# Optimization experiments

Measured on AMD Instinct MI355X. Metric: run time of the kernel, lower is better.

The kernel has to match this reference:

```python
import jax, jax.numpy as jnp
import numpy as np

ACT_BITS = 7      # activation - 1 (symmetric signed quantization)
WEIGHT_BITS = 7   # weight - 1
LN_EPS = 1e-5


def t_quantize(x, k):
    # Symmetric per-tensor uniform quantization to k bits with STE.
    # q = round(clip(x/s, -1, 1) * (2^k - 1)) / (2^k - 1) * s, s = max|x|
    n = float(2 ** k - 1)
    s = jnp.maximum(jnp.max(jnp.abs(x)), 1e-12)
    q = jnp.round(jnp.clip(x / s, -1.0, 1.0) * n) / n * s
    return x + jax.lax.stop_gradient(q - x)  # straight-through


def layer_norm(x, gamma, beta):
    mu = jnp.mean(x, axis=-1, keepdims=True)
    var = jnp.mean(jnp.square(x - mu), axis=-1, keepdims=True)
    return (x - mu) * jax.lax.rsqrt(var + LN_EPS) * gamma + beta


def ir_linear(x, w, b):
    # IRlinear: linear with per-tensor quantized weights (STE).
    wq = t_quantize(w, WEIGHT_BITS)
    return jnp.einsum('bsd,hd->bsh', x, wq) + b


def setup_inputs() -> dict:
    key = jax.random.key(0)
    ks = jax.random.split(key, 4)
    dim, hidden = 1024, 4096
    B, S = 4, 8192
    return {
        'x': jax.random.normal(ks[0], (B, S, dim), dtype=jnp.float32),
        'gamma': jnp.ones((dim,), jnp.float32),
        'beta': jnp.zeros((dim,), jnp.float32),
        'w1': jax.random.normal(ks[1], (hidden, dim), jnp.float32) * (1.0 / np.sqrt(dim)),
        'b1': jnp.zeros((hidden,), jnp.float32),
        'w2': jax.random.normal(ks[2], (dim, hidden), jnp.float32) * (1.0 / np.sqrt(hidden)),
        'b2': jnp.zeros((dim,), jnp.float32),
    }


def reference(x, gamma, beta, w1, b1, w2, b2):
    # x = T_quantize(LayerNorm(x), activation-1)
    h = t_quantize(layer_norm(x, gamma, beta), ACT_BITS)
    # x = T_quantize(GELU(IRlinear1(x)), activation-1)  (exact erf GELU, torch default)
    h = t_quantize(jax.nn.gelu(ir_linear(h, w1, b1), approximate=False), ACT_BITS)
    # net[3:] = Dropout(0) -> IRlinear2 -> Dropout(0)
    return ir_linear(h, w2, b2)
```

## Files before the change

### kernel.cpp

```cpp
#include <hip/hip_runtime.h>
#include <stdint.h>

typedef int v4i __attribute__((ext_vector_type(4)));

#define GLD_LDS16(g, l) __builtin_amdgcn_global_load_lds( \
    (const __attribute__((address_space(1))) void*)(g),   \
    (__attribute__((address_space(3))) void*)(l), 16, 0, 0)

__device__ __forceinline__ float wsum(float v){
  #pragma unroll
  for (int o = 32; o; o >>= 1) v += __shfl_xor(v, o, 64);
  return v;
}
__device__ __forceinline__ float wmaxr(float v){
  #pragma unroll
  for (int o = 32; o; o >>= 1) v = fmaxf(v, __shfl_xor(v, o, 64));
  return v;
}
__device__ __forceinline__ float gelu_f(float x){
  return 0.5f * x * (1.0f + erff(x * 0.7071067811865476f));
}

__global__ __launch_bounds__(256) void k_ln_absmax(
    const float* __restrict__ x, const float* __restrict__ gamma,
    const float* __restrict__ beta, unsigned int* __restrict__ smax_out, int M)
{
  __shared__ float red[4];
  const int lane = threadIdx.x & 63, wave = threadIdx.x >> 6;
  float lmax = 0.f;
  for (int row = blockIdx.x * 4 + wave; row < M; row += gridDim.x * 4) {
    const float4* xr = (const float4*)(x + (size_t)row * 1024);
    float4 v[4]; float s = 0.f;
    #pragma unroll
    for (int j = 0; j < 4; j++){ v[j] = xr[j*64 + lane]; s += v[j].x+v[j].y+v[j].z+v[j].w; }
    s = wsum(s);
    const float mu = s * (1.f/1024.f);
    float sq = 0.f;
    #pragma unroll
    for (int j = 0; j < 4; j++){
      float a=v[j].x-mu, b=v[j].y-mu, c=v[j].z-mu, d=v[j].w-mu;
      sq += a*a + b*b + c*c + d*d;
    }
    sq = wsum(sq);
    const float rs = 1.0f / sqrtf(sq * (1.f/1024.f) + 1e-5f);
    #pragma unroll
    for (int j = 0; j < 4; j++){
      int c0 = j*256 + lane*4;
      float4 g = *(const float4*)(gamma + c0);
      float4 b = *(const float4*)(beta + c0);
      float y0=(v[j].x-mu)*rs*g.x+b.x, y1=(v[j].y-mu)*rs*g.y+b.y;
      float y2=(v[j].z-mu)*rs*g.z+b.z, y3=(v[j].w-mu)*rs*g.w+b.w;
      lmax = fmaxf(lmax, fmaxf(fmaxf(fabsf(y0),fabsf(y1)), fmaxf(fabsf(y2),fabsf(y3))));
    }
  }
  lmax = wmaxr(lmax);
  if (lane == 0) red[wave] = lmax;
  __syncthreads();
  if (threadIdx.x == 0)
    atomicMax(smax_out, __float_as_uint(fmaxf(fmaxf(red[0],red[1]), fmaxf(red[2],red[3]))));
}

__global__ __launch_bounds__(256) void k_ln_quant(
    const float* __restrict__ x, const float* __restrict__ gamma,
    const float* __restrict__ beta, const unsigned int* __restrict__ sbits,
    signed char* __restrict__ A1, int M)
{
  const float s = fmaxf(__uint_as_float(*sbits), 1e-12f);
  const int lane = threadIdx.x & 63, wave = threadIdx.x >> 6;
  for (int row = blockIdx.x * 4 + wave; row < M; row += gridDim.x * 4) {
    const float4* xr = (const float4*)(x + (size_t)row * 1024);
    float4 v[4]; float sm = 0.f;
    #pragma unroll
    for (int j = 0; j < 4; j++){ v[j] = xr[j*64 + lane]; sm += v[j].x+v[j].y+v[j].z+v[j].w; }
    sm = wsum(sm);
    const float mu = sm * (1.f/1024.f);
    float sq = 0.f;
    #pragma unroll
    for (int j = 0; j < 4; j++){
      float a=v[j].x-mu, b=v[j].y-mu, c=v[j].z-mu, d=v[j].w-mu;
      sq += a*a + b*b + c*c + d*d;
    }
    sq = wsum(sq);
    const float rs = 1.0f / sqrtf(sq * (1.f/1024.f) + 1e-5f);
    #pragma unroll
    for (int j = 0; j < 4; j++){
      int c0 = j*256 + lane*4;
      float4 g = *(const float4*)(gamma + c0);
      float4 b = *(const float4*)(beta + c0);
      float y0=(v[j].x-mu)*rs*g.x+b.x, y1=(v[j].y-mu)*rs*g.y+b.y;
      float y2=(v[j].z-mu)*rs*g.z+b.z, y3=(v[j].w-mu)*rs*g.w+b.w;
      char4 qc;
      qc.x = (signed char)(int)rintf(fminf(fmaxf(y0/s,-1.f),1.f)*127.f);
      qc.y = (signed char)(int)rintf(fminf(fmaxf(y1/s,-1.f),1.f)*127.f);
      qc.z = (signed char)(int)rintf(fminf(fmaxf(y2/s,-1.f),1.f)*127.f);
      qc.w = (signed char)(int)rintf(fminf(fmaxf(y3/s,-1.f),1.f)*127.f);
      *(char4*)(A1 + (size_t)row*1024 + c0) = qc;
    }
  }
}

__global__ __launch_bounds__(256) void k_absmax(
    const float* __restrict__ w, long n4, unsigned int* __restrict__ out)
{
  __shared__ float red[4];
  const int lane = threadIdx.x & 63, wave = threadIdx.x >> 6;
  float lmax = 0.f;
  for (long i = blockIdx.x*256 + threadIdx.x; i < n4; i += (long)gridDim.x*256) {
    float4 v = ((const float4*)w)[i];
    lmax = fmaxf(lmax, fmaxf(fmaxf(fabsf(v.x),fabsf(v.y)), fmaxf(fabsf(v.z),fabsf(v.w))));
  }
  lmax = wmaxr(lmax);
  if (lane == 0) red[wave] = lmax;
  __syncthreads();
  if (threadIdx.x == 0)
    atomicMax(out, __float_as_uint(fmaxf(fmaxf(red[0],red[1]), fmaxf(red[2],red[3]))));
}

__global__ __launch_bounds__(256) void k_wquant(
    const float* __restrict__ w, long n4, const unsigned int* __restrict__ sbits,
    signed char* __restrict__ wq)
{
  const float s = fmaxf(__uint_as_float(*sbits), 1e-12f);
  for (long i = blockIdx.x*256 + threadIdx.x; i < n4; i += (long)gridDim.x*256) {
    float4 v = ((const float4*)w)[i];
    char4 qc;
    qc.x = (signed char)(int)rintf(fminf(fmaxf(v.x/s,-1.f),1.f)*127.f);
    qc.y = (signed char)(int)rintf(fminf(fmaxf(v.y/s,-1.f),1.f)*127.f);
    qc.z = (signed char)(int)rintf(fminf(fmaxf(v.z/s,-1.f),1.f)*127.f);
    qc.w = (signed char)(int)rintf(fminf(fmaxf(v.w/s,-1.f),1.f)*127.f);
    *(char4*)(wq + i*4) = qc;
  }
}

template<int MODE>
__global__ __launch_bounds__(256, 4) void k_gemm_i8(
    const signed char* __restrict__ A, const signed char* __restrict__ W,
    const float* __restrict__ bias, const unsigned int* __restrict__ scales,
    float* __restrict__ outf, signed char* __restrict__ outq,
    unsigned int* __restrict__ gmax,
    int M, int N, int K, int ia, int iw, int ig)
{
  __shared__ __align__(16) signed char As[128*64];
  __shared__ __align__(16) signed char Bs[128*64];
  __shared__ float red[4];

  const int nwg = gridDim.x, orig = blockIdx.x;
  const int q8 = nwg >> 3, r8 = nwg & 7;
  const int xcd = orig & 7, idx = orig >> 3;
  const int wgid = (xcd < r8 ? xcd*(q8+1) : r8*(q8+1) + (xcd-r8)*q8) + idx;

  const int tn = N >> 7;
  const int bm = wgid / tn, bn = wgid % tn;
  const int tid = threadIdx.x, lane = tid & 63, wave = tid >> 6;
  const int wm = wave >> 1, wn = wave & 1;
  const size_t row0 = (size_t)bm * 128, col0 = (size_t)bn * 128;

  v4i acc[4][4];
  #pragma unroll
  for (int i = 0; i < 4; i++)
    #pragma unroll
    for (int j = 0; j < 4; j++) acc[i][j] = (v4i){0,0,0,0};

  int st_r[2], st_kk[2];
  #pragma unroll
  for (int i = 0; i < 2; i++) {
    const int chunk = i*4 + wave;
    const int off = chunk*1024 + lane*16;
    const int r = off >> 6;
    const int c = (off >> 4) & 3;
    st_r[i]  = r;
    st_kk[i] = (c ^ ((r >> 1) & 3)) << 4;
  }

  const int ksteps = K >> 6;
  for (int kt = 0; kt < ksteps; ++kt) {
    const size_t kb = (size_t)kt << 6;
    #pragma unroll
    for (int i = 0; i < 2; i++) {
      const int chunk = i*4 + wave;
      GLD_LDS16(A + (row0 + st_r[i])*(size_t)K + kb + st_kk[i], As + chunk*1024);
      GLD_LDS16(W + (col0 + st_r[i])*(size_t)K + kb + st_kk[i], Bs + chunk*1024);
    }
    __syncthreads();

    v4i af[4], bf[4];
    const int cfrag = lane >> 4;
    #pragma unroll
    for (int mi = 0; mi < 4; mi++) {
      const int rr = wm*64 + mi*16 + (lane & 15);
      af[mi] = *(const v4i*)(As + (rr << 6) + ((cfrag ^ ((rr >> 1) & 3)) << 4));
    }
    #pragma unroll
    for (int ni = 0; ni < 4; ni++) {
      const int rr = wn*64 + ni*16 + (lane & 15);
      bf[ni] = *(const v4i*)(Bs + (rr << 6) + ((cfrag ^ ((rr >> 1) & 3)) << 4));
    }
    #pragma unroll
    for (int mi = 0; mi < 4; mi++)
      #pragma unroll
      for (int ni = 0; ni < 4; ni++)
        acc[mi][ni] = __builtin_amdgcn_mfma_i32_16x16x64_i8(af[mi], bf[ni], acc[mi][ni], 0, 0, 0);
    __syncthreads();
  }

  const float sa = fmaxf(__uint_as_float(scales[ia]), 1e-12f);
  const float sw = fmaxf(__uint_as_float(scales[iw]), 1e-12f);
  const float sc = (sa / 127.f) * (sw / 127.f);
  const int rowbase = (int)row0 + wm*64;
  const int colbase = (int)col0 + wn*64;

  if (MODE == 0) {
    float lmax = 0.f;
    #pragma unroll
    for (int mi = 0; mi < 4; mi++)
      #pragma unroll
      for (int ni = 0; ni < 4; ni++) {
        const int colc = colbase + ni*16 + (lane & 15);
        const float b = bias[colc];
        #pragma unroll
        for (int j = 0; j < 4; j++) {
          float g = gelu_f((float)acc[mi][ni][j] * sc + b);
          lmax = fmaxf(lmax, fabsf(g));
        }
      }
    lmax = wmaxr(lmax);
    if (lane == 0) red[wave] = lmax;
    __syncthreads();
    if (tid == 0)
      atomicMax(gmax, __float_as_uint(fmaxf(fmaxf(red[0],red[1]), fmaxf(red[2],red[3]))));
  } else if (MODE == 1) {
    const float sg = fmaxf(__uint_as_float(scales[ig]), 1e-12f);
    #pragma unroll
    for (int mi = 0; mi < 4; mi++)
      #pragma unroll
      for (int ni = 0; ni < 4; ni++) {
        const int colc = colbase + ni*16 + (lane & 15);
        const float b = bias[colc];
        #pragma unroll
        for (int j = 0; j < 4; j++) {
          const int row = rowbase + mi*16 + ((lane >> 4) << 2) + j;
          float g = gelu_f((float)acc[mi][ni][j] * sc + b);
          float t = fminf(fmaxf(g / sg, -1.f), 1.f) * 127.f;
          outq[(size_t)row * N + colc] = (signed char)(int)rintf(t);
        }
      }
  } else {
    #pragma unroll
    for (int mi = 0; mi < 4; mi++)
      #pragma unroll
      for (int ni = 0; ni < 4; ni++) {
        const int colc = colbase + ni*16 + (lane & 15);
        const float b = bias[colc];
        #pragma unroll
        for (int j = 0; j < 4; j++) {
          const int row = rowbase + mi*16 + ((lane >> 4) << 2) + j;
          outf[(size_t)row * N + colc] = (float)acc[mi][ni][j] * sc + b;
        }
      }
  }
}

extern "C" void kernel_launch(void* const* d_in, const int* in_sizes, int n_in,
                              void* d_out, int out_size, void* d_ws, size_t ws_size,
                              hipStream_t stream)
{
  const float* x     = (const float*)d_in[0];
  const float* gamma = (const float*)d_in[1];
  const float* beta  = (const float*)d_in[2];
  const float* w1    = (const float*)d_in[3];
  const float* b1    = (const float*)d_in[4];
  const float* w2    = (const float*)d_in[5];
  const float* b2    = (const float*)d_in[6];
  float* out = (float*)d_out;

  const int D = 1024;
  const int M = in_sizes[0] / D;
  const int H = in_sizes[3] / D;

  char* ws = (char*)d_ws;
  unsigned int* scales = (unsigned int*)ws;
  signed char* A1  = (signed char*)(ws + 256);
  signed char* w1q = A1 + (size_t)M * D;
  signed char* w2q = w1q + (size_t)H * D;
  signed char* A2  = w2q + (size_t)H * D;

  hipMemsetAsync(scales, 0, 32, stream);
  k_absmax<<<512, 256, 0, stream>>>(w1, (long)H * D / 4, scales + 1);
  k_absmax<<<512, 256, 0, stream>>>(w2, (long)H * D / 4, scales + 2);
  k_ln_absmax<<<4096, 256, 0, stream>>>(x, gamma, beta, scales, M);
  k_wquant<<<512, 256, 0, stream>>>(w1, (long)H * D / 4, scales + 1, w1q);
  k_wquant<<<512, 256, 0, stream>>>(w2, (long)H * D / 4, scales + 2, w2q);
  k_ln_quant<<<4096, 256, 0, stream>>>(x, gamma, beta, scales, A1, M);

  const int g1 = (M / 128) * (H / 128);
  k_gemm_i8<0><<<g1, 256, 0, stream>>>(A1, w1q, b1, scales, nullptr, nullptr,
                                       scales + 3, M, H, D, 0, 1, 0);
  k_gemm_i8<1><<<g1, 256, 0, stream>>>(A1, w1q, b1, scales, nullptr, A2,
                                       nullptr, M, H, D, 0, 1, 3);
  const int g2 = (M / 128) * (D / 128);
  k_gemm_i8<2><<<g2, 256, 0, stream>>>(A2, w2q, b2, scales, out, nullptr,
                                       nullptr, M, D, H, 3, 2, 0);
}
```

Measured before the change: 1.182 ms.

## Double-buffer LDS tiles in int8 GEMM to overlap global loads with MFMA

Splits the A and W shared-memory tiles into two buffers. The next K-slice is prefetched with global_load_lds while MFMAs run on the current slice, and the per-iteration barrier pair becomes a single vmcnt wait plus barrier. MFMA sections are wrapped in s_setprio to favour the compute waves. This doubles LDS use per block and lowers the launch-bounds occupancy hint from 4 to 2, which may cut the number of resident waves available to hide latency.

```diff
diff --git a/kernel.cpp b/kernel.cpp
--- a/kernel.cpp
+++ b/kernel.cpp
@@ -133,15 +133,15 @@
 }
 
 template<int MODE>
-__global__ __launch_bounds__(256, 4) void k_gemm_i8(
+__global__ __launch_bounds__(256, 2) void k_gemm_i8(
     const signed char* __restrict__ A, const signed char* __restrict__ W,
     const float* __restrict__ bias, const unsigned int* __restrict__ scales,
     float* __restrict__ outf, signed char* __restrict__ outq,
     unsigned int* __restrict__ gmax,
     int M, int N, int K, int ia, int iw, int ig)
 {
-  __shared__ __align__(16) signed char As[128*64];
-  __shared__ __align__(16) signed char Bs[128*64];
+  __shared__ __align__(16) signed char As[2][128*64];
+  __shared__ __align__(16) signed char Bs[2][128*64];
   __shared__ float red[4];
 
   const int nwg = gridDim.x, orig = blockIdx.x;
@@ -161,7 +161,7 @@
     #pragma unroll
     for (int j = 0; j < 4; j++) acc[i][j] = (v4i){0,0,0,0};
 
-  int st_r[2], st_kk[2];
+  int st_r[2], st_kk[2], st_ch[2];
   #pragma unroll
   for (int i = 0; i < 2; i++) {
     const int chunk = i*4 + wave;
@@ -170,38 +170,55 @@
     const int c = (off >> 4) & 3;
     st_r[i]  = r;
     st_kk[i] = (c ^ ((r >> 1) & 3)) << 4;
-  }
+    st_ch[i] = chunk*1024;
+  }
+  const signed char* Ab = A + row0 * (size_t)K;
+  const signed char* Wb = W + col0 * (size_t)K;
+
+  #define STAGE(buf, kb_) do {                                              \
+    _Pragma("unroll")                                                       \
+    for (int i_ = 0; i_ < 2; i_++) {                                        \
+      GLD_LDS16(Ab + (size_t)st_r[i_]*K + (kb_) + st_kk[i_], As[buf] + st_ch[i_]); \
+      GLD_LDS16(Wb + (size_t)st_r[i_]*K + (kb_) + st_kk[i_], Bs[buf] + st_ch[i_]); \
+    }                                                                       \
+  } while (0)
 
   const int ksteps = K >> 6;
+  STAGE(0, 0);
+  asm volatile("s_waitcnt vmcnt(0)");
+  __builtin_amdgcn_s_barrier();
+
+  int cur = 0;
   for (int kt = 0; kt < ksteps; ++kt) {
-    const size_t kb = (size_t)kt << 6;
-    #pragma unroll
-    for (int i = 0; i < 2; i++) {
-      const int chunk = i*4 + wave;
-      GLD_LDS16(A + (row0 + st_r[i])*(size_t)K + kb + st_kk[i], As + chunk*1024);
-      GLD_LDS16(W + (col0 + st_r[i])*(size_t)K + kb + st_kk[i], Bs + chunk*1024);
-    }
-    __syncthreads();
+    if (kt + 1 < ksteps) STAGE(cur ^ 1, (size_t)(kt + 1) << 6);
 
     v4i af[4], bf[4];
     const int cfrag = lane >> 4;
     #pragma unroll
     for (int mi = 0; mi < 4; mi++) {
       const int rr = wm*64 + mi*16 + (lane & 15);
-      af[mi] = *(const v4i*)(As + (rr << 6) + ((cfrag ^ ((rr >> 1) & 3)) << 4));
+      af[mi] = *(const v4i*)(As[cur] + (rr << 6) + ((cfrag ^ ((rr >> 1) & 3)) << 4));
     }
     #pragma unroll
     for (int ni = 0; ni < 4; ni++) {
       const int rr = wn*64 + ni*16 + (lane & 15);
-      bf[ni] = *(const v4i*)(Bs + (rr << 6) + ((cfrag ^ ((rr >> 1) & 3)) << 4));
-    }
+      bf[ni] = *(const v4i*)(Bs[cur] + (rr << 6) + ((cfrag ^ ((rr >> 1) & 3)) << 4));
+    }
+    __builtin_amdgcn_s_setprio(1);
     #pragma unroll
     for (int mi = 0; mi < 4; mi++)
       #pragma unroll
       for (int ni = 0; ni < 4; ni++)
         acc[mi][ni] = __builtin_amdgcn_mfma_i32_16x16x64_i8(af[mi], bf[ni], acc[mi][ni], 0, 0, 0);
-    __syncthreads();
-  }
+    __builtin_amdgcn_s_setprio(0);
+
+    if (kt + 1 < ksteps) {
+      asm volatile("s_waitcnt vmcnt(0)");
+      __builtin_amdgcn_s_barrier();
+      cur ^= 1;
+    }
+  }
+  #undef STAGE
 
   const float sa = fmaxf(__uint_as_float(scales[ia]), 1e-12f);
   const float sw = fmaxf(__uint_as_float(scales[iw]), 1e-12f);
```

New measurement: 1.044 ms. -11.7%, faster.
